# Kernel tuning notes

Measured on AMD Instinct MI355X. Metric: run time of the kernel, lower is better.

Reference implementation:

```python
import jax, jax.numpy as jnp
import numpy as np

NUM_HEADS = 8

def _feature_map(t):
    return jax.nn.elu(t) + 1.0

def setup_inputs() -> dict:
    key = jax.random.key(0)
    ks = jax.random.split(key, 7)
    B, S, D = 2, 1024, 512
    sc = 1.0 / np.sqrt(D)
    return {
        'x':  jax.random.normal(ks[0], (B, S, D), dtype=jnp.float32),
        'Wq': jax.random.normal(ks[1], (D, D), dtype=jnp.float32) * sc,
        'Wk': jax.random.normal(ks[2], (D, D), dtype=jnp.float32) * sc,
        'Wv': jax.random.normal(ks[3], (D, D), dtype=jnp.float32) * sc,
        'Wo': jax.random.normal(ks[4], (D, D), dtype=jnp.float32) * sc,
        'bo': jnp.zeros((D,), dtype=jnp.float32),
        'Wg': jax.random.normal(ks[5], (2 * D, D), dtype=jnp.float32) * (1.0 / np.sqrt(2 * D)),
        'bg': jnp.zeros((D,), dtype=jnp.float32),
    }

def reference(x, Wq, Wk, Wv, Wo, bo, Wg, bg):
    B, S, D = x.shape
    H = NUM_HEADS
    hd = D // H
    # projections, split heads -> [B,S,H,hd]
    q = _feature_map((x @ Wq).reshape(B, S, H, hd))
    k = _feature_map((x @ Wk).reshape(B, S, H, hd))
    v = (x @ Wv).reshape(B, S, H, hd)
    # causal linear attention via cumulative sums
    kv = jnp.einsum('bshd,bshe->bshde', k, v)        # [B,S,H,hd,hd]
    kv_cumsum = jnp.cumsum(kv, axis=1)
    k_cumsum = jnp.cumsum(k, axis=1)
    numerator = jnp.einsum('bshd,bshde->bshe', q, kv_cumsum)
    denominator = jnp.einsum('bshd,bshd->bsh', q, k_cumsum)[..., None]
    out = (numerator / (denominator + 1e-6)).reshape(B, S, D)
    out = out @ Wo + bo
    gate = jax.nn.sigmoid(jnp.concatenate([x, out], axis=-1) @ Wg + bg)
    return x + gate * (out - x)
```

## Files before the change

kernel.cpp:

```cpp
#include <hip/hip_runtime.h>
#include <hip/hip_bf16.h>
#include <math.h>


typedef __bf16 bf16x8 __attribute__((ext_vector_type(8)));
typedef __bf16 bf16x4 __attribute__((ext_vector_type(4)));
typedef float f32x4 __attribute__((ext_vector_type(4)));

#define MFMA16(a, b, c) __builtin_amdgcn_mfma_f32_16x16x32_bf16(a, b, c, 0, 0, 0)

__device__ __forceinline__ float elu1(float v) { return v > 0.f ? v + 1.f : __expf(v); }

__device__ __forceinline__ void gload16(const void* g, void* l) {
    __builtin_amdgcn_global_load_lds((const __attribute__((address_space(1))) void*)g,
                                     (__attribute__((address_space(3))) void*)l, 16, 0, 0);
}

__global__ __launch_bounds__(256) void prep_kernel(
    const float* __restrict__ x, const float* __restrict__ Wq, const float* __restrict__ Wk,
    const float* __restrict__ Wv, const float* __restrict__ Wo, const float* __restrict__ Wg,
    __bf16* __restrict__ xb, __bf16* __restrict__ wqkvT, __bf16* __restrict__ woT,
    __bf16* __restrict__ wg2T) {
    int z = blockIdx.z;
    if (z == 5) {
        int bid = blockIdx.y * 16 + blockIdx.x;
        int base = (bid * 256 + threadIdx.x) * 8;
        bf16x8 o;
#pragma unroll
        for (int j = 0; j < 8; j++) o[j] = (__bf16)x[base + j];
        *(bf16x8*)&xb[base] = o;
        return;
    }
    const float* in;
    int R = 512;
    if (z == 0) in = Wq;
    else if (z == 1) in = Wk;
    else if (z == 2) in = Wv;
    else if (z == 3) in = Wo;
    else { in = Wg; R = 1024; }
    if ((int)blockIdx.y * 32 >= R) return;
    __shared__ float t[32][33];
    int bx = blockIdx.x, by = blockIdx.y;
    int tx = threadIdx.x & 31, ty = threadIdx.x >> 5;
#pragma unroll
    for (int i = 0; i < 32; i += 8)
        t[ty + i][tx] = in[(size_t)(by * 32 + ty + i) * 512 + bx * 32 + tx];
    __syncthreads();
#pragma unroll
    for (int i = 0; i < 32; i += 8) {
        int n = bx * 32 + ty + i;
        int kk = by * 32 + tx;
        __bf16 val = (__bf16)t[tx][ty + i];
        if (z == 0) wqkvT[(size_t)n * 512 + kk] = val;
        else if (z == 1) wqkvT[(size_t)(512 + n) * 512 + kk] = val;
        else if (z == 2) wqkvT[(size_t)(1024 + n) * 512 + kk] = val;
        else if (z == 3) woT[(size_t)n * 512 + kk] = val;
        else if (kk < 512) wqkvT[(size_t)(1536 + n) * 512 + kk] = val;
        else wg2T[(size_t)n * 512 + (kk - 512)] = val;
    }
}

template <int MODE>
__global__ __launch_bounds__(256) void gemm_kernel(
    const __bf16* __restrict__ A, const __bf16* __restrict__ Bw, const float* __restrict__ bias,
    const float* __restrict__ xf, const __bf16* __restrict__ xgb, const __bf16* __restrict__ pvb,
    float* __restrict__ outf, __bf16* __restrict__ outb,
    __bf16* __restrict__ q_out, __bf16* __restrict__ k_out,
    __bf16* __restrict__ kt_out, __bf16* __restrict__ vt_out, __bf16* __restrict__ xg_out, int K) {
    __shared__ __bf16 sA[3 * 64 * 64];
    __shared__ __bf16 sB[3 * 64 * 64];
    int bm = blockIdx.x, bn = blockIdx.y;
    int tid = threadIdx.x, w = tid >> 6, l = tid & 63;
    int wr = (w >> 1) * 32, wc = (w & 1) * 32;
    f32x4 acc[2][2] = {};
    const int nt = K / 64;

    auto stage = [&](int t, int buf) {
        int k0 = t * 64;
#pragma unroll
        for (int i = 0; i < 2; i++) {
            int row = i * 32 + w * 8 + (l >> 3);
            int gc = (((l & 7) << 4) ^ ((row & 7) << 4)) >> 1;
            gload16(&A[(size_t)(bm * 64 + row) * K + k0 + gc],
                    &sA[buf * 4096 + i * 2048 + w * 512]);
            gload16(&Bw[(size_t)(bn * 64 + row) * K + k0 + gc],
                    &sB[buf * 4096 + i * 2048 + w * 512]);
        }
    };

    stage(0, 0);
    stage(1, 1);
    for (int t = 0; t < nt; t++) {
        if (t + 1 < nt) asm volatile("s_waitcnt vmcnt(4)" ::: "memory");
        else asm volatile("s_waitcnt vmcnt(0)" ::: "memory");
        asm volatile("s_barrier" ::: "memory");
        if (t + 2 < nt) stage(t + 2, (t + 2) % 3);
        int buf = t % 3;
        bf16x8 af[2][2], bfr[2][2];
#pragma unroll
        for (int kk = 0; kk < 2; kk++) {
            int cb = kk * 64 + ((l >> 4) << 4);
#pragma unroll
            for (int mi = 0; mi < 2; mi++) {
                int rowA = wr + mi * 16 + (l & 15);
                af[kk][mi] = *(const bf16x8*)&sA[buf * 4096 + rowA * 64 +
                                                ((cb ^ ((rowA & 7) << 4)) >> 1)];
            }
#pragma unroll
            for (int ni = 0; ni < 2; ni++) {
                int rowB = wc + ni * 16 + (l & 15);
                bfr[kk][ni] = *(const bf16x8*)&sB[buf * 4096 + rowB * 64 +
                                                 ((cb ^ ((rowB & 7) << 4)) >> 1)];
            }
        }
#pragma unroll
        for (int kk = 0; kk < 2; kk++)
#pragma unroll
            for (int mi = 0; mi < 2; mi++)
#pragma unroll
                for (int ni = 0; ni < 2; ni++)
                    acc[mi][ni] = MFMA16(af[kk][mi], bfr[kk][ni], acc[mi][ni]);
    }

    if (MODE == 0) {
        __bf16* sE = sA;
        __syncthreads();
#pragma unroll
        for (int mi = 0; mi < 2; mi++)
#pragma unroll
            for (int ni = 0; ni < 2; ni++)
#pragma unroll
                for (int j = 0; j < 4; j++) {
                    int lr = wr + mi * 16 + ((l >> 4) << 2) + j;
                    int lc = wc + ni * 16 + (l & 15);
                    float v = acc[mi][ni][j];
                    if (bn < 16) v = elu1(v);
                    sE[lr * 72 + lc] = (__bf16)v;
                }
        __syncthreads();
        int which = bn >> 3;
        int b = bm >> 4, s0b = (bm & 15) * 64, h = bn & 7;
        int bh = b * 8 + h;
        if (which == 0 || which == 1) {
            __bf16* qk = (which == 0 ? q_out : k_out) + ((size_t)(bh * 1024 + s0b)) * 64;
#pragma unroll
            for (int p = 0; p < 2; p++) {
                int idx = p * 256 + tid;
                *(bf16x8*)&qk[idx * 8] = *(const bf16x8*)&sE[(idx >> 3) * 72 + (idx & 7) * 8];
            }
        }
        if (which == 1 || which == 2) {
            __bf16* tdst = (which == 1 ? kt_out : vt_out) + (size_t)(bh * 64) * 1024 + s0b;
            alignas(16) __bf16 tmp[16];
#pragma unroll
            for (int sj = 0; sj < 16; sj++) tmp[sj] = sE[(w * 16 + sj) * 72 + l];
            *(bf16x8*)&tdst[(size_t)l * 1024 + w * 16] = *(const bf16x8*)&tmp[0];
            *(bf16x8*)&tdst[(size_t)l * 1024 + w * 16 + 8] = *(const bf16x8*)&tmp[8];
        }
        if (which == 3) {
            __bf16* dst = xg_out + (size_t)(bm * 64) * 512 + (bn - 24) * 64;
#pragma unroll
            for (int p = 0; p < 2; p++) {
                int idx = p * 256 + tid;
                *(bf16x8*)&dst[(size_t)(idx >> 3) * 512 + (idx & 7) * 8] =
                    *(const bf16x8*)&sE[(idx >> 3) * 72 + (idx & 7) * 8];
            }
        }
    } else {
#pragma unroll
        for (int mi = 0; mi < 2; mi++)
#pragma unroll
            for (int ni = 0; ni < 2; ni++)
#pragma unroll
                for (int j = 0; j < 4; j++) {
                    int gm = bm * 64 + wr + mi * 16 + ((l >> 4) << 2) + j;
                    int gn = bn * 64 + wc + ni * 16 + (l & 15);
                    if (MODE == 1) {
                        float v = acc[mi][ni][j] + bias[gn];
                        outb[(size_t)gm * 512 + gn] = (__bf16)v;
                    } else {
                        float v = acc[mi][ni][j] + (float)xgb[(size_t)gm * 512 + gn] + bias[gn];
                        float g = 1.f / (1.f + __expf(-v));
                        float xv = xf[(size_t)gm * 512 + gn];
                        float pv = (float)pvb[(size_t)gm * 512 + gn];
                        outf[(size_t)gm * 512 + gn] = xv + g * (pv - xv);
                    }
                }
    }
}

__global__ __launch_bounds__(256) void mc_kernel(const __bf16* __restrict__ ktb,
                                                 const __bf16* __restrict__ vtb,
                                                 float* __restrict__ Mc, float* __restrict__ ksc) {
    int blk = blockIdx.x;
    int bh = blk >> 3, ch = blk & 7;
    int tid = threadIdx.x, w = tid >> 6, l = tid & 63;
    const __bf16* vb = vtb + (size_t)bh * 65536 + ch * 128;
    const __bf16* kp = ktb + (size_t)bh * 65536 + ch * 128;
    f32x4 macc[4] = {};
#pragma unroll
    for (int ks = 0; ks < 4; ks++) {
        bf16x8 a = *(const bf16x8*)&vb[(size_t)(w * 16 + (l & 15)) * 1024 + ks * 32 + ((l >> 4) << 3)];
#pragma unroll
        for (int ni = 0; ni < 4; ni++) {
            bf16x8 bb = *(const bf16x8*)&kp[(size_t)(ni * 16 + (l & 15)) * 1024 + ks * 32 + ((l >> 4) << 3)];
            macc[ni] = MFMA16(a, bb, macc[ni]);
        }
    }
    float* mout = Mc + (size_t)blk * 4096;
#pragma unroll
    for (int ni = 0; ni < 4; ni++)
#pragma unroll
        for (int j = 0; j < 4; j++)
            mout[(size_t)(w * 16 + ((l >> 4) << 2) + j) * 64 + ni * 16 + (l & 15)] = macc[ni][j];
    if (tid < 64) {
        float s = 0.f;
        const __bf16* kr = ktb + (size_t)(bh * 64 + tid) * 1024 + ch * 128;
#pragma unroll
        for (int t = 0; t < 16; t++) {
            bf16x8 v = *(const bf16x8*)&kr[t * 8];
#pragma unroll
            for (int j = 0; j < 8; j++) s += (float)v[j];
        }
        ksc[blk * 64 + tid] = s;
    }
}

__global__ __launch_bounds__(256) void attn_kernel(
    const __bf16* __restrict__ qb, const __bf16* __restrict__ kb,
    const __bf16* __restrict__ vtb, const float* __restrict__ Mc,
    const float* __restrict__ ksc, __bf16* __restrict__ attn_out) {
    int blk = blockIdx.x;
    int bh = blk >> 4, ch = (blk >> 1) & 7, half = blk & 1;
    int b = bh >> 3, h = bh & 7;
    int tid = threadIdx.x, w = tid >> 6, l = tid & 63;

    __shared__ __bf16 sQ[64 * 72];
    __shared__ __bf16 sP[64 * 136];
    __shared__ __bf16 sM[64 * 72];
    __shared__ float den[64];
    __shared__ float rsum[64];
    __shared__ float ksst[64];

    const __bf16* qsrc = qb + (size_t)(bh * 1024 + ch * 128 + half * 64) * 64;
#pragma unroll
    for (int i = 0; i < 2; i++) {
        int e = i * 2048 + tid * 8;
        *(bf16x8*)&sQ[(e >> 6) * 72 + (e & 63)] = *(const bf16x8*)&qsrc[e];
    }
    {
        int r0 = tid >> 2, c0 = (tid & 3) * 16;
        f32x4 s0 = {}, s1 = {}, s2 = {}, s3 = {};
        const float* mcb = Mc + (size_t)(bh * 8) * 4096 + r0 * 64 + c0;
        for (int c = 0; c < ch; c++) {
            const float* p = mcb + (size_t)c * 4096;
            s0 += *(const f32x4*)&p[0];
            s1 += *(const f32x4*)&p[4];
            s2 += *(const f32x4*)&p[8];
            s3 += *(const f32x4*)&p[12];
        }
        __bf16* d = &sM[r0 * 72 + c0];
#pragma unroll
        for (int j = 0; j < 4; j++) {
            d[j] = (__bf16)s0[j];
            d[4 + j] = (__bf16)s1[j];
            d[8 + j] = (__bf16)s2[j];
            d[12 + j] = (__bf16)s3[j];
        }
    }
    if (tid < 64) {
        float s = 0.f;
        for (int c = 0; c < ch; c++) s += ksc[(bh * 8 + c) * 64 + tid];
        ksst[tid] = s;
    }
    __syncthreads();

    if (tid < 64) {
        float s = 0.f;
#pragma unroll
        for (int d0 = 0; d0 < 64; d0 += 8) {
            bf16x8 qv = *(const bf16x8*)&sQ[tid * 72 + d0];
#pragma unroll
            for (int jj = 0; jj < 8; jj++) s += (float)qv[jj] * ksst[d0 + jj];
        }
        den[tid] = s;
    }

    {
        int wr = w * 16;
        const int CFMAX = half ? (w + 4) : w;
        const int CFLIM = half ? 7 : 3;
        const __bf16* kbase = kb + (size_t)(bh * 1024 + ch * 128) * 64;
        bf16x8 aq[2];
#pragma unroll
        for (int ks = 0; ks < 2; ks++)
            aq[ks] = *(const bf16x8*)&sQ[(wr + (l & 15)) * 72 + ks * 32 + ((l >> 4) << 3)];
        f32x4 acc[8] = {};
#pragma unroll
        for (int cf = 0; cf < 8; cf++) {
            if (cf <= CFMAX && cf <= CFLIM) {
#pragma unroll
                for (int ks = 0; ks < 2; ks++) {
                    bf16x8 bfr = *(const bf16x8*)&kbase[(size_t)(cf * 16 + (l & 15)) * 64 + ks * 32 + ((l >> 4) << 3)];
                    acc[cf] = MFMA16(aq[ks], bfr, acc[cf]);
                }
            }
        }
#pragma unroll
        for (int j = 0; j < 4; j++) {
            int lrow = wr + ((l >> 4) << 2) + j;
            int grow = half * 64 + lrow;
            float rs = 0.f;
#pragma unroll
            for (int cf = 0; cf < 8; cf++) {
                if (cf <= CFMAX && cf <= CFLIM) {
                    int col = cf * 16 + (l & 15);
                    float v = acc[cf][j];
                    v = (col <= grow) ? v : 0.f;
                    rs += v;
                    sP[lrow * 136 + col] = (__bf16)v;
                }
            }
            if (CFMAX + 1 <= CFLIM) sP[lrow * 136 + (CFMAX + 1) * 16 + (l & 15)] = (__bf16)0.f;
#pragma unroll
            for (int off = 1; off < 16; off <<= 1) rs += __shfl_xor(rs, off);
            if ((l & 15) == 0) rsum[lrow] = rs;
        }
    }
    __syncthreads();

    f32x4 o[4] = {};
    {
        int wr = w * 16;
        int ksmax = half ? (2 + (w >> 1)) : (w >> 1);
        const __bf16* vbase = vtb + (size_t)bh * 65536 + ch * 128;
#pragma unroll
        for (int ks = 0; ks < 4; ks++) {
            if (ks <= ksmax) {
                bf16x8 a = *(const bf16x8*)&sP[(wr + (l & 15)) * 136 + ks * 32 + ((l >> 4) << 3)];
#pragma unroll
                for (int ni = 0; ni < 4; ni++) {
                    bf16x8 bfr = *(const bf16x8*)&vbase[(size_t)(ni * 16 + (l & 15)) * 1024 + ks * 32 + ((l >> 4) << 3)];
                    o[ni] = MFMA16(a, bfr, o[ni]);
                }
            }
        }
        if (ch > 0) {
#pragma unroll
            for (int ks = 0; ks < 2; ks++) {
                bf16x8 a = *(const bf16x8*)&sQ[(wr + (l & 15)) * 72 + ks * 32 + ((l >> 4) << 3)];
#pragma unroll
                for (int ni = 0; ni < 4; ni++) {
                    bf16x8 bfr = *(const bf16x8*)&sM[(ni * 16 + (l & 15)) * 72 + ks * 32 + ((l >> 4) << 3)];
                    o[ni] = MFMA16(a, bfr, o[ni]);
                }
            }
        }
    }

    __bf16* obase = attn_out + ((size_t)(b * 1024 + ch * 128 + half * 64)) * 512 + h * 64;
#pragma unroll
    for (int j = 0; j < 4; j++) {
        int lrow = w * 16 + ((l >> 4) << 2) + j;
        float dn = den[lrow] + rsum[lrow] + 1e-6f;
#pragma unroll
        for (int ni = 0; ni < 4; ni++) {
            int col = ni * 16 + (l & 15);
            obase[(size_t)lrow * 512 + col] = (__bf16)(o[ni][j] / dn);
        }
    }
}

extern "C" void kernel_launch(void* const* d_in, const int* in_sizes, int n_in,
                              void* d_out, int out_size, void* d_ws, size_t ws_size,
                              hipStream_t stream) {
    const float* x = (const float*)d_in[0];
    const float* Wq = (const float*)d_in[1];
    const float* Wk = (const float*)d_in[2];
    const float* Wv = (const float*)d_in[3];
    const float* Wo = (const float*)d_in[4];
    const float* bo = (const float*)d_in[5];
    const float* Wg = (const float*)d_in[6];
    const float* bg = (const float*)d_in[7];
    float* out = (float*)d_out;

    char* ws = (char*)d_ws;
    size_t off = 0;
    auto alloc = [&](size_t bytes) -> void* {
        void* p = ws + off;
        off += (bytes + 255) & ~(size_t)255;
        return p;
    };
    __bf16* xb    = (__bf16*)alloc((size_t)2048 * 512 * 2);
    __bf16* wqkvT = (__bf16*)alloc((size_t)2048 * 512 * 2);
    __bf16* woT   = (__bf16*)alloc((size_t)512 * 512 * 2);
    __bf16* wg2T  = (__bf16*)alloc((size_t)512 * 512 * 2);
    __bf16* qb    = (__bf16*)alloc((size_t)16 * 1024 * 64 * 2);
    __bf16* kb    = (__bf16*)alloc((size_t)16 * 1024 * 64 * 2);
    __bf16* ktb   = (__bf16*)alloc((size_t)16 * 64 * 1024 * 2);
    __bf16* vtb   = (__bf16*)alloc((size_t)16 * 64 * 1024 * 2);
    float*  Mc    = (float*)alloc((size_t)128 * 4096 * 4);
    float*  ksc   = (float*)alloc((size_t)128 * 64 * 4);
    __bf16* attn  = (__bf16*)alloc((size_t)2048 * 512 * 2);
    __bf16* projb = (__bf16*)alloc((size_t)2048 * 512 * 2);
    __bf16* xgb   = (__bf16*)alloc((size_t)2048 * 512 * 2);

    prep_kernel<<<dim3(16, 32, 6), 256, 0, stream>>>(x, Wq, Wk, Wv, Wo, Wg, xb, wqkvT, woT, wg2T);
    gemm_kernel<0><<<dim3(32, 32), 256, 0, stream>>>(
        xb, wqkvT, nullptr, nullptr, nullptr, nullptr, nullptr, nullptr,
        qb, kb, ktb, vtb, xgb, 512);
    mc_kernel<<<128, 256, 0, stream>>>(ktb, vtb, Mc, ksc);
    attn_kernel<<<256, 256, 0, stream>>>(qb, kb, vtb, Mc, ksc, attn);
    gemm_kernel<1><<<dim3(32, 8), 256, 0, stream>>>(
        attn, woT, bo, nullptr, nullptr, nullptr, nullptr, projb,
        nullptr, nullptr, nullptr, nullptr, nullptr, 512);
    gemm_kernel<2><<<dim3(32, 8), 256, 0, stream>>>(
        projb, wg2T, bg, x, xgb, projb, out, nullptr,
        nullptr, nullptr, nullptr, nullptr, nullptr, 512);
}
```

Before: 58.12 us.

## Use dedicated 128x128-tile QKV projection kernel with 512 threads

Replaces the MODE 0 path of the generic 64x64 GEMM with a dedicated kernel that computes 128x128 output tiles using 8 waves and double-buffered LDS staging. The epilogue is rewritten to scatter two heads per block into the q, k, transposed k/v and gate-x buffers. Larger tiles raise data reuse and cut the launch from 1024 to 256 blocks, which fill the CUs less evenly. Fewer pipeline stages (2 instead of 3) may expose more load latency.

Result: faster. 54.70 us (-5.9%).

```diff
diff --git a/kernel.cpp b/kernel.cpp
--- a/kernel.cpp
+++ b/kernel.cpp
@@ -60,13 +60,121 @@
     }
 }
 
+__global__ __launch_bounds__(512) void qkv_kernel(
+    const __bf16* __restrict__ A, const __bf16* __restrict__ Bw,
+    __bf16* __restrict__ q_out, __bf16* __restrict__ k_out,
+    __bf16* __restrict__ kt_out, __bf16* __restrict__ vt_out, __bf16* __restrict__ xg_out) {
+    __shared__ __bf16 smem[32768];
+    __bf16* sA = smem;
+    __bf16* sB = smem + 16384;
+    int bm = blockIdx.x, bn = blockIdx.y;
+    int tid = threadIdx.x, w = tid >> 6, l = tid & 63;
+    int wr = (w >> 2) * 64, wc = (w & 3) * 32;
+    f32x4 acc[4][2] = {};
+    const int nt = 8;
+
+    auto stage = [&](int t, int buf) {
+        int k0 = t * 64;
+#pragma unroll
+        for (int i = 0; i < 2; i++) {
+            int row = i * 64 + w * 8 + (l >> 3);
+            int gc = (((l & 7) << 4) ^ ((row & 7) << 4)) >> 1;
+            gload16(&A[(size_t)(bm * 128 + row) * 512 + k0 + gc],
+                    &sA[buf * 8192 + i * 4096 + w * 512]);
+            gload16(&Bw[(size_t)(bn * 128 + row) * 512 + k0 + gc],
+                    &sB[buf * 8192 + i * 4096 + w * 512]);
+        }
+    };
+
+    stage(0, 0);
+    for (int t = 0; t < nt; t++) {
+        asm volatile("s_waitcnt vmcnt(0)" ::: "memory");
+        asm volatile("s_barrier" ::: "memory");
+        if (t + 1 < nt) stage(t + 1, (t + 1) & 1);
+        int buf = t & 1;
+#pragma unroll
+        for (int kk = 0; kk < 2; kk++) {
+            int cb = kk * 64 + ((l >> 4) << 4);
+            bf16x8 af[4], bfr[2];
+#pragma unroll
+            for (int mi = 0; mi < 4; mi++) {
+                int rowA = wr + mi * 16 + (l & 15);
+                af[mi] = *(const bf16x8*)&sA[buf * 8192 + rowA * 64 +
+                                            ((cb ^ ((rowA & 7) << 4)) >> 1)];
+            }
+#pragma unroll
+            for (int ni = 0; ni < 2; ni++) {
+                int rowB = wc + ni * 16 + (l & 15);
+                bfr[ni] = *(const bf16x8*)&sB[buf * 8192 + rowB * 64 +
+                                             ((cb ^ ((rowB & 7) << 4)) >> 1)];
+            }
+#pragma unroll
+            for (int mi = 0; mi < 4; mi++)
+#pragma unroll
+                for (int ni = 0; ni < 2; ni++)
+                    acc[mi][ni] = MFMA16(af[mi], bfr[ni], acc[mi][ni]);
+        }
+    }
+
+    __bf16* sE = smem;
+    __syncthreads();
+#pragma unroll
+    for (int mi = 0; mi < 4; mi++)
+#pragma unroll
+        for (int ni = 0; ni < 2; ni++)
+#pragma unroll
+            for (int j = 0; j < 4; j++) {
+                int lr = wr + mi * 16 + ((l >> 4) << 2) + j;
+                int lc = wc + ni * 16 + (l & 15);
+                float v = acc[mi][ni][j];
+                if (bn < 8) v = elu1(v);
+                sE[lr * 136 + lc] = (__bf16)v;
+            }
+    __syncthreads();
+    int which = bn >> 2;
+    int h0 = (bn & 3) * 2;
+    int b = bm >> 3, s0b = (bm & 7) * 128;
+    int bh0 = b * 8 + h0;
+    if (which == 0 || which == 1) {
+        __bf16* qk = (which == 0 ? q_out : k_out);
+#pragma unroll
+        for (int p = 0; p < 4; p++) {
+            int idx = p * 512 + tid;
+            int token = idx >> 4, colv = idx & 15;
+            int c2 = colv >> 3, d8 = (colv & 7) * 8;
+            *(bf16x8*)&qk[((size_t)((bh0 + c2) * 1024 + s0b + token)) * 64 + d8] =
+                *(const bf16x8*)&sE[token * 136 + colv * 8];
+        }
+    }
+    if (which == 1 || which == 2) {
+        __bf16* tbase = (which == 1 ? kt_out : vt_out);
+#pragma unroll
+        for (int c2 = 0; c2 < 2; c2++) {
+            alignas(16) __bf16 tmp[16];
+#pragma unroll
+            for (int sj = 0; sj < 16; sj++) tmp[sj] = sE[(w * 16 + sj) * 136 + c2 * 64 + l];
+            __bf16* tdst = tbase + ((size_t)((bh0 + c2) * 64 + l)) * 1024 + s0b + w * 16;
+            *(bf16x8*)&tdst[0] = *(const bf16x8*)&tmp[0];
+            *(bf16x8*)&tdst[8] = *(const bf16x8*)&tmp[8];
+        }
+    }
+    if (which == 3) {
+        __bf16* dst = xg_out + (size_t)(bm * 128) * 512 + (bn & 3) * 128;
+#pragma unroll
+        for (int p = 0; p < 4; p++) {
+            int idx = p * 512 + tid;
+            int token = idx >> 4, colv = idx & 15;
+            *(bf16x8*)&dst[(size_t)token * 512 + colv * 8] =
+                *(const bf16x8*)&sE[token * 136 + colv * 8];
+        }
+    }
+}
+
 template <int MODE>
 __global__ __launch_bounds__(256) void gemm_kernel(
     const __bf16* __restrict__ A, const __bf16* __restrict__ Bw, const float* __restrict__ bias,
     const float* __restrict__ xf, const __bf16* __restrict__ xgb, const __bf16* __restrict__ pvb,
-    float* __restrict__ outf, __bf16* __restrict__ outb,
-    __bf16* __restrict__ q_out, __bf16* __restrict__ k_out,
-    __bf16* __restrict__ kt_out, __bf16* __restrict__ vt_out, __bf16* __restrict__ xg_out, int K) {
+    float* __restrict__ outf, __bf16* __restrict__ outb, int K) {
     __shared__ __bf16 sA[3 * 64 * 64];
     __shared__ __bf16 sB[3 * 64 * 64];
     int bm = blockIdx.x, bn = blockIdx.y;
@@ -122,71 +230,25 @@
                     acc[mi][ni] = MFMA16(af[kk][mi], bfr[kk][ni], acc[mi][ni]);
     }
 
-    if (MODE == 0) {
-        __bf16* sE = sA;
-        __syncthreads();
-#pragma unroll
-        for (int mi = 0; mi < 2; mi++)
-#pragma unroll
-            for (int ni = 0; ni < 2; ni++)
-#pragma unroll
-                for (int j = 0; j < 4; j++) {
-                    int lr = wr + mi * 16 + ((l >> 4) << 2) + j;
-                    int lc = wc + ni * 16 + (l & 15);
-                    float v = acc[mi][ni][j];
-                    if (bn < 16) v = elu1(v);
-                    sE[lr * 72 + lc] = (__bf16)v;
+#pragma unroll
+    for (int mi = 0; mi < 2; mi++)
+#pragma unroll
+        for (int ni = 0; ni < 2; ni++)
+#pragma unroll
+            for (int j = 0; j < 4; j++) {
+                int gm = bm * 64 + wr + mi * 16 + ((l >> 4) << 2) + j;
+                int gn = bn * 64 + wc + ni * 16 + (l & 15);
+                if (MODE == 1) {
+                    float v = acc[mi][ni][j] + bias[gn];
+                    outb[(size_t)gm * 512 + gn] = (__bf16)v;
+                } else {
+                    float v = acc[mi][ni][j] + (float)xgb[(size_t)gm * 512 + gn] + bias[gn];
+                    float g = 1.f / (1.f + __expf(-v));
+                    float xv = xf[(size_t)gm * 512 + gn];
+                    float pv = (float)pvb[(size_t)gm * 512 + gn];
+                    outf[(size_t)gm * 512 + gn] = xv + g * (pv - xv);
                 }
-        __syncthreads();
-        int which = bn >> 3;
-        int b = bm >> 4, s0b = (bm & 15) * 64, h = bn & 7;
-        int bh = b * 8 + h;
-        if (which == 0 || which == 1) {
-            __bf16* qk = (which == 0 ? q_out : k_out) + ((size_t)(bh * 1024 + s0b)) * 64;
-#pragma unroll
-            for (int p = 0; p < 2; p++) {
-                int idx = p * 256 + tid;
-                *(bf16x8*)&qk[idx * 8] = *(const bf16x8*)&sE[(idx >> 3) * 72 + (idx & 7) * 8];
-            }
-        }
-        if (which == 1 || which == 2) {
-            __bf16* tdst = (which == 1 ? kt_out : vt_out) + (size_t)(bh * 64) * 1024 + s0b;
-            alignas(16) __bf16 tmp[16];
-#pragma unroll
-            for (int sj = 0; sj < 16; sj++) tmp[sj] = sE[(w * 16 + sj) * 72 + l];
-            *(bf16x8*)&tdst[(size_t)l * 1024 + w * 16] = *(const bf16x8*)&tmp[0];
-            *(bf16x8*)&tdst[(size_t)l * 1024 + w * 16 + 8] = *(const bf16x8*)&tmp[8];
-        }
-        if (which == 3) {
-            __bf16* dst = xg_out + (size_t)(bm * 64) * 512 + (bn - 24) * 64;
-#pragma unroll
-            for (int p = 0; p < 2; p++) {
-                int idx = p * 256 + tid;
-                *(bf16x8*)&dst[(size_t)(idx >> 3) * 512 + (idx & 7) * 8] =
-                    *(const bf16x8*)&sE[(idx >> 3) * 72 + (idx & 7) * 8];
-            }
-        }
-    } else {
-#pragma unroll
-        for (int mi = 0; mi < 2; mi++)
-#pragma unroll
-            for (int ni = 0; ni < 2; ni++)
-#pragma unroll
-                for (int j = 0; j < 4; j++) {
-                    int gm = bm * 64 + wr + mi * 16 + ((l >> 4) << 2) + j;
-                    int gn = bn * 64 + wc + ni * 16 + (l & 15);
-                    if (MODE == 1) {
-                        float v = acc[mi][ni][j] + bias[gn];
-                        outb[(size_t)gm * 512 + gn] = (__bf16)v;
-                    } else {
-                        float v = acc[mi][ni][j] + (float)xgb[(size_t)gm * 512 + gn] + bias[gn];
-                        float g = 1.f / (1.f + __expf(-v));
-                        float xv = xf[(size_t)gm * 512 + gn];
-                        float pv = (float)pvb[(size_t)gm * 512 + gn];
-                        outf[(size_t)gm * 512 + gn] = xv + g * (pv - xv);
-                    }
-                }
-    }
+            }
 }
 
 __global__ __launch_bounds__(256) void mc_kernel(const __bf16* __restrict__ ktb,
@@ -406,15 +468,11 @@
     __bf16* xgb   = (__bf16*)alloc((size_t)2048 * 512 * 2);
 
     prep_kernel<<<dim3(16, 32, 6), 256, 0, stream>>>(x, Wq, Wk, Wv, Wo, Wg, xb, wqkvT, woT, wg2T);
-    gemm_kernel<0><<<dim3(32, 32), 256, 0, stream>>>(
-        xb, wqkvT, nullptr, nullptr, nullptr, nullptr, nullptr, nullptr,
-        qb, kb, ktb, vtb, xgb, 512);
+    qkv_kernel<<<dim3(16, 16), 512, 0, stream>>>(xb, wqkvT, qb, kb, ktb, vtb, xgb);
     mc_kernel<<<128, 256, 0, stream>>>(ktb, vtb, Mc, ksc);
     attn_kernel<<<256, 256, 0, stream>>>(qb, kb, vtb, Mc, ksc, attn);
     gemm_kernel<1><<<dim3(32, 8), 256, 0, stream>>>(
-        attn, woT, bo, nullptr, nullptr, nullptr, nullptr, projb,
-        nullptr, nullptr, nullptr, nullptr, nullptr, 512);
+        attn, woT, bo, nullptr, nullptr, nullptr, nullptr, projb, 512);
     gemm_kernel<2><<<dim3(32, 8), 256, 0, stream>>>(
-        projb, wg2T, bg, x, xgb, projb, out, nullptr,
-        nullptr, nullptr, nullptr, nullptr, nullptr, 512);
-}
+        projb, wg2T, bg, x, xgb, projb, out, nullptr, 512);
+}
```
